# Kernel optimization log

Hardware: AMD Instinct MI355X
Metric: run time of the kernel (lower is better)

Reference implementation:

```python
import jax, jax.numpy as jnp
import numpy as np

B, S, D, H, E, TOP_K = 8, 2048, 2048, 2048, 4, 2


def setup_inputs() -> dict:
    key = jax.random.key(0)
    ks = jax.random.split(key, 6)
    scale = 0.02
    return {
        "hidden_states": jax.random.normal(ks[0], (B, S, D), jnp.float32),
        "gate_w": jax.random.normal(ks[1], (E, D), jnp.float32) * scale,  # Linear(D -> E), no bias
        "w1": jax.random.normal(ks[2], (E, D, H), jnp.float32) * scale,   # per-expert Linear(D -> H)
        "b1": jnp.zeros((E, H), jnp.float32),
        "w2": jax.random.normal(ks[3], (E, H, H), jnp.float32) * scale,   # per-expert Linear(H -> H)
        "b2": jnp.zeros((E, H), jnp.float32),
    }


def reference(hidden_states, gate_w, w1, b1, w2, b2):
    b, s, d = hidden_states.shape
    x = hidden_states.reshape(-1, d)                       # [N, D]
    n = x.shape[0]

    # Router: softmax in fp32, top-k, renormalize (matches torch forward)
    logits = jnp.einsum("nd,ed->ne", x, gate_w)            # [N, E]
    rw = jax.nn.softmax(logits.astype(jnp.float32), axis=-1)
    top_w, sel = jax.lax.top_k(rw, TOP_K)                  # [N, K]
    top_w = top_w / jnp.sum(top_w, axis=-1, keepdims=True)
    top_w = top_w.astype(x.dtype)

    # Scatter top-k weights back to a dense [N, E] combine matrix
    w_full = jnp.zeros((n, E), x.dtype).at[jnp.arange(n)[:, None], sel].set(top_w)

    # Per-expert FFN: Linear -> exact GELU -> Linear (dense over all tokens,
    # combined with zero weight for unselected experts == gather/scatter math)
    h1 = jax.nn.gelu(jnp.einsum("nd,edh->enh", x, w1) + b1[:, None, :], approximate=False)
    out_e = jnp.einsum("enh,eho->eno", h1, w2) + b2[:, None, :]  # [E, N, H]

    out = jnp.einsum("eno,ne->no", out_e, w_full)          # weighted combine
    return out.reshape(b, s, -1)
```

## Files before the change

kernel.cpp:

```cpp
#include <hip/hip_runtime.h>
#include <hip/hip_bf16.h>
#include <math.h>

typedef __bf16 bf16x8 __attribute__((ext_vector_type(8)));
typedef __bf16 bf16x4 __attribute__((ext_vector_type(4)));
typedef float f32x4 __attribute__((ext_vector_type(4)));

typedef __attribute__((address_space(1))) void GV;
typedef __attribute__((address_space(3))) void LV;

template <int OSTRIDE, bool EBLOCK>
__global__ __launch_bounds__(256) void transpose_cvt(const float* __restrict__ in,
                                                     __bf16* __restrict__ out) {
  __shared__ float tile[32][33];
  const int e = blockIdx.z;
  const size_t ibase = (size_t)e * 2048 * 2048;
  const size_t obase = EBLOCK ? (size_t)e * 2048 * 2048 : (size_t)e * 2048;
  int c0 = blockIdx.x * 32, r0 = blockIdx.y * 32;
  int tx = threadIdx.x & 31, ty = threadIdx.x >> 5;
#pragma unroll
  for (int i = 0; i < 32; i += 8)
    tile[ty + i][tx] = in[ibase + (size_t)(r0 + ty + i) * 2048 + c0 + tx];
  __syncthreads();
#pragma unroll
  for (int i = 0; i < 32; i += 8)
    out[obase + (size_t)(c0 + ty + i) * OSTRIDE + r0 + tx] = (__bf16)tile[tx][ty + i];
}

__global__ __launch_bounds__(256) void router_fused(const float4* __restrict__ hs4,
                                                    const float4* __restrict__ gw4,
                                                    bf16x4* __restrict__ xb,
                                                    float* __restrict__ comb,
                                                    int* __restrict__ pairid,
                                                    int* __restrict__ cnt) {
  __shared__ float4 gwS[4 * 512];
  const int tid = threadIdx.x;
  for (int j = tid; j < 2048; j += 256) gwS[j] = gw4[j];
  __syncthreads();

  const int lane = tid & 63;
  const int wv = tid >> 6;
  const int nA = blockIdx.x * 8 + wv * 2;
  const int nB = nA + 1;

  const float4* xA = hs4 + (size_t)nA * 512;
  const float4* xB = hs4 + (size_t)nB * 512;
  bf16x4* dA = xb + (size_t)nA * 512;
  bf16x4* dB = xb + (size_t)nB * 512;

  float4 va[8], vb[8];
#pragma unroll
  for (int i = 0; i < 8; ++i) va[i] = xA[i * 64 + lane];
#pragma unroll
  for (int i = 0; i < 8; ++i) vb[i] = xB[i * 64 + lane];

  float a0 = 0.f, a1 = 0.f, a2 = 0.f, a3 = 0.f;
  float c0 = 0.f, c1 = 0.f, c2 = 0.f, c3 = 0.f;
#pragma unroll
  for (int i = 0; i < 8; ++i) {
    int j = i * 64 + lane;
    float4 g0 = gwS[j], g1 = gwS[512 + j], g2 = gwS[1024 + j], g3 = gwS[1536 + j];
    float4 v = va[i];
    a0 += v.x * g0.x + v.y * g0.y + v.z * g0.z + v.w * g0.w;
    a1 += v.x * g1.x + v.y * g1.y + v.z * g1.z + v.w * g1.w;
    a2 += v.x * g2.x + v.y * g2.y + v.z * g2.z + v.w * g2.w;
    a3 += v.x * g3.x + v.y * g3.y + v.z * g3.z + v.w * g3.w;
    bf16x4 oa;
    oa.x = (__bf16)v.x; oa.y = (__bf16)v.y; oa.z = (__bf16)v.z; oa.w = (__bf16)v.w;
    dA[j] = oa;
    float4 w = vb[i];
    c0 += w.x * g0.x + w.y * g0.y + w.z * g0.z + w.w * g0.w;
    c1 += w.x * g1.x + w.y * g1.y + w.z * g1.z + w.w * g1.w;
    c2 += w.x * g2.x + w.y * g2.y + w.z * g2.z + w.w * g2.w;
    c3 += w.x * g3.x + w.y * g3.y + w.z * g3.z + w.w * g3.w;
    bf16x4 ob;
    ob.x = (__bf16)w.x; ob.y = (__bf16)w.y; ob.z = (__bf16)w.z; ob.w = (__bf16)w.w;
    dB[j] = ob;
  }

#pragma unroll
  for (int off = 32; off > 0; off >>= 1) {
    a0 += __shfl_xor(a0, off); a1 += __shfl_xor(a1, off);
    a2 += __shfl_xor(a2, off); a3 += __shfl_xor(a3, off);
    c0 += __shfl_xor(c0, off); c1 += __shfl_xor(c1, off);
    c2 += __shfl_xor(c2, off); c3 += __shfl_xor(c3, off);
  }

  if (lane < 2) {
    const int n = lane ? nB : nA;
    float l[4];
    l[0] = lane ? c0 : a0; l[1] = lane ? c1 : a1;
    l[2] = lane ? c2 : a2; l[3] = lane ? c3 : a3;
    float m = fmaxf(fmaxf(l[0], l[1]), fmaxf(l[2], l[3]));
    float p[4], sum = 0.f;
#pragma unroll
    for (int e = 0; e < 4; ++e) { p[e] = expf(l[e] - m); sum += p[e]; }
#pragma unroll
    for (int e = 0; e < 4; ++e) p[e] /= sum;
    int i1 = 0;
#pragma unroll
    for (int e = 1; e < 4; ++e) if (p[e] > p[i1]) i1 = e;
    int i2 = -1;
#pragma unroll
    for (int e = 0; e < 4; ++e) {
      if (e == i1) continue;
      if (i2 < 0 || p[e] > p[i2]) i2 = e;
    }
    float ws = p[i1] + p[i2];
#pragma unroll
    for (int e = 0; e < 4; ++e)
      comb[(size_t)n * 4 + e] = (e == i1 || e == i2) ? p[e] / ws : 0.f;
    int a = min(i1, i2), b = max(i1, i2);
    int pid = (a == 0) ? (b - 1) : ((a == 1) ? (1 + b) : (2 + b));
    pairid[n] = pid;
    atomicAdd(&cnt[pid], 1);
  }
}

__global__ void scan6(const int* __restrict__ cnt, int* __restrict__ off) {
  int o = 0;
  for (int i = 0; i < 6; ++i) { off[i] = o; o += cnt[i]; }
}

__global__ __launch_bounds__(256) void assign_kernel(const int* __restrict__ pairid,
                                                     const float4* __restrict__ comb4,
                                                     const int* __restrict__ off,
                                                     int* __restrict__ cur,
                                                     int* __restrict__ perm,
                                                     float4* __restrict__ comb_s,
                                                     int* __restrict__ pm_s) {
  int n = blockIdx.x * 256 + threadIdx.x;
  int pid = pairid[n];
  int pos = off[pid] + atomicAdd(&cur[pid], 1);
  perm[pos] = n;
  comb_s[pos] = comb4[n];
  const int lut[6] = {3, 5, 9, 6, 10, 12};
  pm_s[pos] = lut[pid];
}

__global__ void tile_mask_kernel(const int* __restrict__ pm_s, int* __restrict__ tmask) {
  int t = threadIdx.x;
  int m = 0;
  for (int i = 0; i < 128; ++i) m |= pm_s[t * 128 + i];
  tmask[t] = m;
}

template <int MODE>
__global__ __launch_bounds__(256) void gemm_bt(const __bf16* __restrict__ A,
                                               const __bf16* __restrict__ Bt,
                                               const float* __restrict__ bias,
                                               const float* __restrict__ cc,
                                               const int* __restrict__ tmask,
                                               const int* __restrict__ permc,
                                               void* __restrict__ outp) {
  constexpr int K = (MODE == 0) ? 2048 : 8192;
  __shared__ __bf16 ldsA[128 * 32];
  __shared__ __bf16 ldsB[128 * 32];

  const int tid = threadIdx.x;
  const int lane = tid & 63;
  const int wv = tid >> 6;
  const int bx = blockIdx.x, by = blockIdx.y;

  const int tm = tmask[by];
  if (MODE == 0) {
    if (!(tm & (1 << (bx >> 4)))) return;
  }

  const int lrow = lane & 15;
  const int quad = lane >> 4;
  const int mbase = (wv >> 1) * 64;
  const int nbase = (wv & 1) * 64;

  size_t aoff[2], boff[2];
#pragma unroll
  for (int t = 0; t < 2; ++t) {
    int g = t * 256 + wv * 64 + lane;
    int row = g >> 2, kc = g & 3;
    int arow = by * 128 + row;
    if (MODE == 0) arow = permc[arow];
    aoff[t] = (size_t)arow * K + kc * 8;
    boff[t] = (size_t)(bx * 128 + row) * K + kc * 8;
  }

  f32x4 acc[4][4] = {};

  auto k_step = [&](int kb) {
    __syncthreads();
#pragma unroll
    for (int t = 0; t < 2; ++t) {
      const __bf16* ga = A + aoff[t] + (size_t)kb * 32;
      const __bf16* gb = Bt + boff[t] + (size_t)kb * 32;
      int loff = t * 2048 + wv * 512;
      __builtin_amdgcn_global_load_lds((GV*)ga, (LV*)&ldsA[loff], 16, 0, 0);
      __builtin_amdgcn_global_load_lds((GV*)gb, (LV*)&ldsB[loff], 16, 0, 0);
    }
    __syncthreads();

    bf16x8 af[4], bfr[4];
#pragma unroll
    for (int i = 0; i < 4; ++i)
      af[i] = *(const bf16x8*)&ldsA[(mbase + i * 16 + lrow) * 32 + quad * 8];
#pragma unroll
    for (int i = 0; i < 4; ++i)
      bfr[i] = *(const bf16x8*)&ldsB[(nbase + i * 16 + lrow) * 32 + quad * 8];
#pragma unroll
    for (int mi = 0; mi < 4; ++mi)
#pragma unroll
      for (int ni = 0; ni < 4; ++ni)
        acc[mi][ni] = __builtin_amdgcn_mfma_f32_16x16x32_bf16(af[mi], bfr[ni],
                                                              acc[mi][ni], 0, 0, 0);
  };

  if (MODE == 0) {
    for (int kb = 0; kb < K / 32; ++kb) k_step(kb);
  } else {
    for (int e = 0; e < 4; ++e) {
      if (!(tm & (1 << e))) continue;
      for (int kb = e * 64; kb < e * 64 + 64; ++kb) k_step(kb);
    }
  }

  if (MODE == 0) {
    __bf16* out = (__bf16*)outp;
#pragma unroll
    for (int mi = 0; mi < 4; ++mi) {
#pragma unroll
      for (int ni = 0; ni < 4; ++ni) {
        int gcol = bx * 128 + nbase + ni * 16 + lrow;
        int e = gcol >> 11;
        int h = gcol & 2047;
        float b = bias[e * 2048 + h];
        f32x4 v = acc[mi][ni];
#pragma unroll
        for (int r = 0; r < 4; ++r) {
          int row = by * 128 + mbase + mi * 16 + quad * 4 + r;
          float xv = v[r] + b;
          float gl = 0.5f * xv * (1.0f + erff(xv * 0.70710678118654752440f));
          out[(size_t)row * 8192 + gcol] = (__bf16)(gl * cc[row * 4 + e]);
        }
      }
    }
  } else {
    float* out = (float*)outp;
    float bb[4][4];
#pragma unroll
    for (int ni = 0; ni < 4; ++ni) {
      int gcol = bx * 128 + nbase + ni * 16 + lrow;
#pragma unroll
      for (int e = 0; e < 4; ++e) bb[ni][e] = bias[e * 2048 + gcol];
    }
#pragma unroll
    for (int mi = 0; mi < 4; ++mi) {
#pragma unroll
      for (int r = 0; r < 4; ++r) {
        int row = by * 128 + mbase + mi * 16 + quad * 4 + r;
        int tok = permc[row];
        const float* cw = cc + (size_t)row * 4;
        float c0 = cw[0], c1 = cw[1], c2 = cw[2], c3 = cw[3];
#pragma unroll
        for (int ni = 0; ni < 4; ++ni) {
          int gcol = bx * 128 + nbase + ni * 16 + lrow;
          float s = acc[mi][ni][r] + c0 * bb[ni][0] + c1 * bb[ni][1] +
                    c2 * bb[ni][2] + c3 * bb[ni][3];
          out[(size_t)tok * 2048 + gcol] = s;
        }
      }
    }
  }
}

extern "C" void kernel_launch(void* const* d_in, const int* in_sizes, int n_in,
                              void* d_out, int out_size, void* d_ws, size_t ws_size,
                              hipStream_t stream) {
  const float* hs = (const float*)d_in[0];
  const float* gate_w = (const float*)d_in[1];
  const float* w1 = (const float*)d_in[2];
  const float* b1 = (const float*)d_in[3];
  const float* w2 = (const float*)d_in[4];
  const float* b2 = (const float*)d_in[5];
  float* out = (float*)d_out;

  const int N = 16384, D = 2048, H = 2048, E = 4;

  char* p = (char*)d_ws;
  __bf16* xb = (__bf16*)p;    p += (size_t)N * D * 2;
  __bf16* w1t = (__bf16*)p;   p += (size_t)E * D * H * 2;
  __bf16* w2t = (__bf16*)p;   p += (size_t)E * H * H * 2;
  float* comb = (float*)p;    p += (size_t)N * 4 * 4;
  float* comb_s = (float*)p;  p += (size_t)N * 4 * 4;
  int* perm = (int*)p;        p += (size_t)N * 4;
  int* pairid = (int*)p;      p += (size_t)N * 4;
  int* pm_s = (int*)p;        p += (size_t)N * 4;
  int* meta = (int*)p;        p += 32 * 4;
  int* tmask = (int*)p;       p += 128 * 4;
  __bf16* h1s = (__bf16*)p;

  size_t used = (size_t)(p - (char*)d_ws);
  int CHUNK = 4096;
  if (ws_size >= used + (size_t)16384 * 8192 * 2) CHUNK = 16384;
  else if (ws_size >= used + (size_t)8192 * 8192 * 2) CHUNK = 8192;

  hipMemsetAsync(meta, 0, 64, stream);
  transpose_cvt<2048, true><<<dim3(64, 64, 4), 256, 0, stream>>>(w1, w1t);
  transpose_cvt<8192, false><<<dim3(64, 64, 4), 256, 0, stream>>>(w2, w2t);
  router_fused<<<dim3(N / 8), 256, 0, stream>>>((const float4*)hs,
                                                (const float4*)gate_w,
                                                (bf16x4*)xb, comb, pairid, meta);
  scan6<<<1, 1, 0, stream>>>(meta, meta + 16);
  assign_kernel<<<dim3(N / 256), 256, 0, stream>>>(pairid, (const float4*)comb,
                                                   meta + 16, meta + 8, perm,
                                                   (float4*)comb_s, pm_s);
  tile_mask_kernel<<<1, 128, 0, stream>>>(pm_s, tmask);

  for (int c = 0; c < N / CHUNK; ++c) {
    const float* cc = comb_s + (size_t)c * CHUNK * 4;
    const int* tmc = tmask + c * (CHUNK / 128);
    gemm_bt<0><<<dim3(E * H / 128, CHUNK / 128), 256, 0, stream>>>(
        xb, w1t, b1, cc, tmc, perm + c * CHUNK, h1s);
    gemm_bt<1><<<dim3(H / 128, CHUNK / 128), 256, 0, stream>>>(h1s, w2t, b2, cc, tmc,
                                                               perm + c * CHUNK, out);
  }
}
```

Measured before the change: 1.456 ms.

## Rewrite expert GEMMs with 256x256 tiles, double-buffered swizzled LDS and 8 waves

Replaces the 128x128 single-buffered GEMM with a 256x256-tile, 512-thread kernel that uses a 64-wide K step, XOR-swizzled LDS layout, and double buffering. The next tile's global->LDS loads are interleaved with MFMA quadrants under barriers and s_setprio. Tile masks are recomputed at 256-row granularity, and the second GEMM loops only over active experts. This aims to raise arithmetic intensity and hide load latency, at the cost of coarser expert skipping, larger LDS use (128KB) and lower occupancy.

```diff
diff --git a/kernel.cpp b/kernel.cpp
--- a/kernel.cpp
+++ b/kernel.cpp
@@ -141,12 +141,12 @@
 __global__ void tile_mask_kernel(const int* __restrict__ pm_s, int* __restrict__ tmask) {
   int t = threadIdx.x;
   int m = 0;
-  for (int i = 0; i < 128; ++i) m |= pm_s[t * 128 + i];
+  for (int i = 0; i < 256; ++i) m |= pm_s[t * 256 + i];
   tmask[t] = m;
 }
 
 template <int MODE>
-__global__ __launch_bounds__(256) void gemm_bt(const __bf16* __restrict__ A,
+__global__ __launch_bounds__(512) void gemm256(const __bf16* __restrict__ A,
                                                const __bf16* __restrict__ Bt,
                                                const float* __restrict__ bias,
                                                const float* __restrict__ cc,
@@ -154,87 +154,151 @@
                                                const int* __restrict__ permc,
                                                void* __restrict__ outp) {
   constexpr int K = (MODE == 0) ? 2048 : 8192;
-  __shared__ __bf16 ldsA[128 * 32];
-  __shared__ __bf16 ldsB[128 * 32];
+  __shared__ __attribute__((aligned(128))) __bf16 lds[65536];
 
   const int tid = threadIdx.x;
-  const int lane = tid & 63;
-  const int wv = tid >> 6;
+  const int lane = tid & 63, wv = tid >> 6;
+  const int wm = wv >> 2, wn = wv & 3;
+  const int lrow = lane & 15, quad = lane >> 4;
   const int bx = blockIdx.x, by = blockIdx.y;
 
   const int tm = tmask[by];
+  if (MODE == 0 && !(tm & (1 << (bx >> 3)))) return;
+
+  int nt, aep = 0;
   if (MODE == 0) {
-    if (!(tm & (1 << (bx >> 4)))) return;
-  }
-
-  const int lrow = lane & 15;
-  const int quad = lane >> 4;
-  const int mbase = (wv >> 1) * 64;
-  const int nbase = (wv & 1) * 64;
-
-  size_t aoff[2], boff[2];
-#pragma unroll
-  for (int t = 0; t < 2; ++t) {
-    int g = t * 256 + wv * 64 + lane;
-    int row = g >> 2, kc = g & 3;
-    int arow = by * 128 + row;
+    nt = K / 64;
+  } else {
+    int na = 0;
+    for (int e = 0; e < 4; ++e)
+      if (tm & (1 << e)) { aep |= e << (na * 8); ++na; }
+    nt = na * 32;
+  }
+  auto kb_of = [&](int t) -> int {
+    return (MODE == 0) ? t : ((aep >> ((t >> 5) * 8)) & 7) * 32 + (t & 31);
+  };
+
+  const __bf16* asrc[4];
+  const __bf16* bsrc[4];
+  int lofA[4], lofB[4];
+#pragma unroll
+  for (int i = 0; i < 4; ++i) {
+    int c = i * 512 + tid;
+    int row = c >> 3, cc8 = (c & 7) ^ (row & 7);
+    int arow = by * 256 + row;
     if (MODE == 0) arow = permc[arow];
-    aoff[t] = (size_t)arow * K + kc * 8;
-    boff[t] = (size_t)(bx * 128 + row) * K + kc * 8;
-  }
-
-  f32x4 acc[4][4] = {};
-
-  auto k_step = [&](int kb) {
-    __syncthreads();
-#pragma unroll
-    for (int t = 0; t < 2; ++t) {
-      const __bf16* ga = A + aoff[t] + (size_t)kb * 32;
-      const __bf16* gb = Bt + boff[t] + (size_t)kb * 32;
-      int loff = t * 2048 + wv * 512;
-      __builtin_amdgcn_global_load_lds((GV*)ga, (LV*)&ldsA[loff], 16, 0, 0);
-      __builtin_amdgcn_global_load_lds((GV*)gb, (LV*)&ldsB[loff], 16, 0, 0);
-    }
-    __syncthreads();
-
-    bf16x8 af[4], bfr[4];
+    asrc[i] = A + (size_t)arow * K + cc8 * 8;
+    bsrc[i] = Bt + (size_t)(bx * 256 + row) * K + cc8 * 8;
+    lofA[i] = (i * 512 + wv * 64) * 8;
+    lofB[i] = 32768 + (i * 512 + wv * 64) * 8;
+  }
+
+  auto stageA = [&](int nbuf, int kb) {
 #pragma unroll
     for (int i = 0; i < 4; ++i)
-      af[i] = *(const bf16x8*)&ldsA[(mbase + i * 16 + lrow) * 32 + quad * 8];
+      __builtin_amdgcn_global_load_lds((GV*)(asrc[i] + (size_t)kb * 64),
+                                       (LV*)&lds[nbuf * 16384 + lofA[i]], 16, 0, 0);
+  };
+  auto stageB = [&](int nbuf, int kb) {
 #pragma unroll
     for (int i = 0; i < 4; ++i)
-      bfr[i] = *(const bf16x8*)&ldsB[(nbase + i * 16 + lrow) * 32 + quad * 8];
-#pragma unroll
-    for (int mi = 0; mi < 4; ++mi)
-#pragma unroll
-      for (int ni = 0; ni < 4; ++ni)
-        acc[mi][ni] = __builtin_amdgcn_mfma_f32_16x16x32_bf16(af[mi], bfr[ni],
-                                                              acc[mi][ni], 0, 0, 0);
+      __builtin_amdgcn_global_load_lds((GV*)(bsrc[i] + (size_t)kb * 64),
+                                       (LV*)&lds[nbuf * 16384 + lofB[i]], 16, 0, 0);
   };
 
-  if (MODE == 0) {
-    for (int kb = 0; kb < K / 32; ++kb) k_step(kb);
-  } else {
-    for (int e = 0; e < 4; ++e) {
-      if (!(tm & (1 << e))) continue;
-      for (int kb = e * 64; kb < e * 64 + 64; ++kb) k_step(kb);
-    }
-  }
+  const int aoff = wm * 8192 + lrow * 64;
+  const int boff = wn * 4096 + lrow * 64;
+  const int sk0 = (quad ^ (lrow & 7)) * 8;
+  const int sk1 = ((4 + quad) ^ (lrow & 7)) * 8;
+
+  f32x4 acc[8][4] = {};
+  bf16x8 af[4][2];
+  bf16x8 bfr[2][2][2];
+
+#define LDA_FRAGS(MH)                                                          \
+  _Pragma("unroll") for (int m = 0; m < 4; ++m) {                              \
+    af[m][0] = *(const bf16x8*)&lds[cb16 + aoff + (MH)*4096 + m * 1024 + sk0]; \
+    af[m][1] = *(const bf16x8*)&lds[cb16 + aoff + (MH)*4096 + m * 1024 + sk1]; \
+  }
+#define LDB_FRAGS(NH)                                                          \
+  _Pragma("unroll") for (int n = 0; n < 2; ++n) {                              \
+    bfr[NH][n][0] =                                                            \
+        *(const bf16x8*)&lds[32768 + cb16 + boff + (NH)*2048 + n * 1024 + sk0];\
+    bfr[NH][n][1] =                                                            \
+        *(const bf16x8*)&lds[32768 + cb16 + boff + (NH)*2048 + n * 1024 + sk1];\
+  }
+#define BARRIER_LGKM                                                           \
+  __builtin_amdgcn_s_barrier();                                                \
+  asm volatile("s_waitcnt lgkmcnt(0)" ::: "memory");                           \
+  __builtin_amdgcn_sched_barrier(0);
+#define MFMA_Q(MH, NH)                                                         \
+  __builtin_amdgcn_s_setprio(1);                                               \
+  _Pragma("unroll") for (int m = 0; m < 4; ++m)                                \
+      _Pragma("unroll") for (int n = 0; n < 2; ++n) {                          \
+    acc[(MH)*4 + m][(NH)*2 + n] = __builtin_amdgcn_mfma_f32_16x16x32_bf16(     \
+        af[m][0], bfr[NH][n][0], acc[(MH)*4 + m][(NH)*2 + n], 0, 0, 0);        \
+    acc[(MH)*4 + m][(NH)*2 + n] = __builtin_amdgcn_mfma_f32_16x16x32_bf16(     \
+        af[m][1], bfr[NH][n][1], acc[(MH)*4 + m][(NH)*2 + n], 0, 0, 0);        \
+  }                                                                            \
+  __builtin_amdgcn_s_setprio(0);
+
+  {
+    int kb0 = kb_of(0);
+    stageA(0, kb0);
+    stageB(0, kb0);
+  }
+  asm volatile("s_waitcnt vmcnt(0)" ::: "memory");
+  __builtin_amdgcn_s_barrier();
+
+  for (int t = 0; t < nt; ++t) {
+    const int cb16 = (t & 1) * 16384;
+    const int nbuf = (t & 1) ^ 1;
+    const bool more = (t + 1) < nt;
+    const int kbn = more ? kb_of(t + 1) : 0;
+
+    LDA_FRAGS(0)
+    LDB_FRAGS(0)
+    if (more) stageA(nbuf, kbn);
+    BARRIER_LGKM
+    MFMA_Q(0, 0)
+    __builtin_amdgcn_s_barrier();
+
+    LDB_FRAGS(1)
+    if (more) stageB(nbuf, kbn);
+    BARRIER_LGKM
+    MFMA_Q(0, 1)
+    __builtin_amdgcn_s_barrier();
+
+    LDA_FRAGS(1)
+    BARRIER_LGKM
+    MFMA_Q(1, 1)
+    __builtin_amdgcn_s_barrier();
+
+    BARRIER_LGKM
+    MFMA_Q(1, 0)
+    asm volatile("s_waitcnt vmcnt(0)" ::: "memory");
+    __builtin_amdgcn_s_barrier();
+  }
+
+#undef LDA_FRAGS
+#undef LDB_FRAGS
+#undef BARRIER_LGKM
+#undef MFMA_Q
 
   if (MODE == 0) {
     __bf16* out = (__bf16*)outp;
 #pragma unroll
-    for (int mi = 0; mi < 4; ++mi) {
-#pragma unroll
-      for (int ni = 0; ni < 4; ++ni) {
-        int gcol = bx * 128 + nbase + ni * 16 + lrow;
+    for (int mq = 0; mq < 8; ++mq) {
+#pragma unroll
+      for (int nq = 0; nq < 4; ++nq) {
+        int gcol = bx * 256 + wn * 64 + nq * 16 + lrow;
         int e = gcol >> 11;
         int h = gcol & 2047;
         float b = bias[e * 2048 + h];
-        f32x4 v = acc[mi][ni];
+        f32x4 v = acc[mq][nq];
 #pragma unroll
         for (int r = 0; r < 4; ++r) {
-          int row = by * 128 + mbase + mi * 16 + quad * 4 + r;
+          int row = by * 256 + wm * 128 + mq * 16 + quad * 4 + r;
           float xv = v[r] + b;
           float gl = 0.5f * xv * (1.0f + erff(xv * 0.70710678118654752440f));
           out[(size_t)row * 8192 + gcol] = (__bf16)(gl * cc[row * 4 + e]);
@@ -245,24 +309,24 @@
     float* out = (float*)outp;
     float bb[4][4];
 #pragma unroll
-    for (int ni = 0; ni < 4; ++ni) {
-      int gcol = bx * 128 + nbase + ni * 16 + lrow;
-#pragma unroll
-      for (int e = 0; e < 4; ++e) bb[ni][e] = bias[e * 2048 + gcol];
+    for (int nq = 0; nq < 4; ++nq) {
+      int gcol = bx * 256 + wn * 64 + nq * 16 + lrow;
+#pragma unroll
+      for (int e = 0; e < 4; ++e) bb[nq][e] = bias[e * 2048 + gcol];
     }
 #pragma unroll
-    for (int mi = 0; mi < 4; ++mi) {
+    for (int mq = 0; mq < 8; ++mq) {
 #pragma unroll
       for (int r = 0; r < 4; ++r) {
-        int row = by * 128 + mbase + mi * 16 + quad * 4 + r;
+        int row = by * 256 + wm * 128 + mq * 16 + quad * 4 + r;
         int tok = permc[row];
         const float* cw = cc + (size_t)row * 4;
         float c0 = cw[0], c1 = cw[1], c2 = cw[2], c3 = cw[3];
 #pragma unroll
-        for (int ni = 0; ni < 4; ++ni) {
-          int gcol = bx * 128 + nbase + ni * 16 + lrow;
-          float s = acc[mi][ni][r] + c0 * bb[ni][0] + c1 * bb[ni][1] +
-                    c2 * bb[ni][2] + c3 * bb[ni][3];
+        for (int nq = 0; nq < 4; ++nq) {
+          int gcol = bx * 256 + wn * 64 + nq * 16 + lrow;
+          float s = acc[mq][nq][r] + c0 * bb[nq][0] + c1 * bb[nq][1] +
+                    c2 * bb[nq][2] + c3 * bb[nq][3];
           out[(size_t)tok * 2048 + gcol] = s;
         }
       }
@@ -293,7 +357,7 @@
   int* pairid = (int*)p;      p += (size_t)N * 4;
   int* pm_s = (int*)p;        p += (size_t)N * 4;
   int* meta = (int*)p;        p += 32 * 4;
-  int* tmask = (int*)p;       p += 128 * 4;
+  int* tmask = (int*)p;       p += 64 * 4;
   __bf16* h1s = (__bf16*)p;
 
   size_t used = (size_t)(p - (char*)d_ws);
@@ -311,14 +375,14 @@
   assign_kernel<<<dim3(N / 256), 256, 0, stream>>>(pairid, (const float4*)comb,
                                                    meta + 16, meta + 8, perm,
                                                    (float4*)comb_s, pm_s);
-  tile_mask_kernel<<<1, 128, 0, stream>>>(pm_s, tmask);
+  tile_mask_kernel<<<1, 64, 0, stream>>>(pm_s, tmask);
 
   for (int c = 0; c < N / CHUNK; ++c) {
     const float* cc = comb_s + (size_t)c * CHUNK * 4;
-    const int* tmc = tmask + c * (CHUNK / 128);
-    gemm_bt<0><<<dim3(E * H / 128, CHUNK / 128), 256, 0, stream>>>(
+    const int* tmc = tmask + c * (CHUNK / 256);
+    gemm256<0><<<dim3(E * H / 256, CHUNK / 256), 512, 0, stream>>>(
         xb, w1t, b1, cc, tmc, perm + c * CHUNK, h1s);
-    gemm_bt<1><<<dim3(H / 128, CHUNK / 128), 256, 0, stream>>>(h1s, w2t, b2, cc, tmc,
-                                                               perm + c * CHUNK, out);
-  }
-}
+    gemm256<1><<<dim3(H / 256, CHUNK / 256), 512, 0, stream>>>(
+        h1s, w2t, b2, cc, tmc, perm + c * CHUNK, out);
+  }
+}
```

Measured after the change: 1.441 ms. No clear change (-1.1%).
